# Kernel tuning notes

Measured on AMD Instinct MI355X. Metric: run time of the kernel, lower is better.

The kernel has to match this reference:

```python
import jax, jax.numpy as jnp
import numpy as np
import math

SEQ, BATCH, IN_DIM = 2048, 2, 512
EMBED, HEADS = 512, 8
HEAD_DIM = EMBED // HEADS


def setup_inputs() -> dict:
    key = jax.random.key(0)
    ks = jax.random.split(key, 6)
    # xavier-uniform style init for weights (stored as [in, out])
    def xavier(k, fan_in, fan_out):
        limit = math.sqrt(6.0 / (fan_in + fan_out))
        return jax.random.uniform(k, (fan_in, fan_out), jnp.float32, -limit, limit)
    return {
        "x": jax.random.normal(ks[0], (SEQ, BATCH, IN_DIM), jnp.float32),
        "relative_positional_bias": jax.random.normal(ks[1], (1, HEADS, SEQ, SEQ), jnp.float32),
        "Wqkv": xavier(ks[2], IN_DIM, 3 * EMBED),
        "bqkv": jnp.zeros((3 * EMBED,), jnp.float32),
        "Wo": xavier(ks[3], EMBED, EMBED),
        "bo": jnp.zeros((EMBED,), jnp.float32),
    }


def reference(x, relative_positional_bias, Wqkv, bqkv, Wo, bo):
    # x: [S, B, D] -> [B, S, D]
    xb = jnp.transpose(x, (1, 0, 2))
    B, S, _ = xb.shape
    qkv = xb @ Wqkv + bqkv                       # [B, S, 3E]
    qkv = qkv.reshape(B, S, HEADS, 3 * HEAD_DIM).transpose(0, 2, 1, 3)  # [B,H,S,3hd]
    q, k, v = jnp.split(qkv, 3, axis=-1)         # each [B, H, S, hd]
    # nonstandard scaling: 1/sqrt(2 * d_k)
    scale = 1.0 / math.sqrt(2.0 * HEAD_DIM)
    logits = jnp.einsum("bhqd,bhkd->bhqk", q, k) * scale
    logits = logits + relative_positional_bias   # broadcast over batch
    attn = jax.nn.softmax(logits, axis=-1)
    vals = jnp.einsum("bhqk,bhkd->bhqd", attn, v)  # [B, H, S, hd]
    vals = vals.transpose(0, 2, 1, 3).reshape(B, S, EMBED)
    return vals @ Wo + bo                        # [B, S, E]
```

## Files before the change

### kernel.cpp

```cpp
#include <hip/hip_runtime.h>
#include <hip/hip_bf16.h>

#define SEQ 2048
#define BATCH 2
#define IN_DIM 512
#define EMBED 512
#define HEADS 8
#define HD 64
#define N3 1536

using f32x4 = __attribute__((ext_vector_type(4))) float;
using s16x8 = __attribute__((ext_vector_type(8))) short;

__device__ __forceinline__ unsigned short f2bf(float f) {
    union { float f; unsigned int u; } v; v.f = f;
    unsigned int u = v.u;
    unsigned int r = (u + 0x7FFFu + ((u >> 16) & 1u)) >> 16;
    return (unsigned short)r;
}

__global__ __launch_bounds__(256) void qkv_proj(
    const float* __restrict__ x, const float* __restrict__ Wqkv,
    const float* __restrict__ bqkv,
    unsigned short* __restrict__ Qb, unsigned short* __restrict__ Kb,
    unsigned short* __restrict__ Vt)
{
    __shared__ __align__(16) unsigned short As[64][72];
    __shared__ __align__(16) unsigned short Bs[64][72];
    const int bm = blockIdx.x, bn = blockIdx.y;
    const int tid = threadIdx.x;
    const int lane = tid & 63, w = tid >> 6;
    const int fr = lane & 15, fg = lane >> 4;
    const int m0 = bm * 64, n0 = bn * 64;
    const int ri = tid >> 2;
    const int cj = (tid & 3) * 16;

    f32x4 acc[4];
#pragma unroll
    for (int t = 0; t < 4; t++) acc[t] = (f32x4){0.f, 0.f, 0.f, 0.f};

    const int gm = m0 + ri;
    const int b_ = gm >> 11, s_ = gm & 2047;
    const float* xrow = x + ((size_t)s_ * BATCH + b_) * IN_DIM;

    for (int k0 = 0; k0 < IN_DIM; k0 += 64) {
        {
            const float4* src = reinterpret_cast<const float4*>(xrow + k0 + cj);
#pragma unroll
            for (int v = 0; v < 4; v++) {
                float4 f = src[v];
                ushort4 u;
                u.x = f2bf(f.x); u.y = f2bf(f.y); u.z = f2bf(f.z); u.w = f2bf(f.w);
                *reinterpret_cast<ushort4*>(&As[ri][cj + 4 * v]) = u;
            }
        }
        {
            const float4* src = reinterpret_cast<const float4*>(Wqkv + (size_t)(k0 + ri) * N3 + n0 + cj);
#pragma unroll
            for (int v = 0; v < 4; v++) {
                float4 f = src[v];
                Bs[cj + 4 * v + 0][ri] = f2bf(f.x);
                Bs[cj + 4 * v + 1][ri] = f2bf(f.y);
                Bs[cj + 4 * v + 2][ri] = f2bf(f.z);
                Bs[cj + 4 * v + 3][ri] = f2bf(f.w);
            }
        }
        __syncthreads();
#pragma unroll
        for (int h2 = 0; h2 < 2; h2++) {
            s16x8 a = *reinterpret_cast<const s16x8*>(&As[w * 16 + fr][h2 * 32 + fg * 8]);
#pragma unroll
            for (int t = 0; t < 4; t++) {
                s16x8 b = *reinterpret_cast<const s16x8*>(&Bs[t * 16 + fr][h2 * 32 + fg * 8]);
                acc[t] = __builtin_amdgcn_mfma_f32_16x16x32_bf16(a, b, acc[t], 0, 0, 0);
            }
        }
        __syncthreads();
    }

#pragma unroll
    for (int t = 0; t < 4; t++) {
        const int col = n0 + t * 16 + fr;
        const int h = col / 192, r = col % 192;
        const float bq = bqkv[col];
#pragma unroll
        for (int j = 0; j < 4; j++) {
            const int grow = m0 + w * 16 + fg * 4 + j;
            const int bo_ = grow >> 11, so_ = grow & 2047;
            const unsigned short bv = f2bf(acc[t][j] + bq);
            if (r < 64)
                Qb[(((size_t)bo_ * HEADS + h) * SEQ + so_) * HD + r] = bv;
            else if (r < 128)
                Kb[(((size_t)bo_ * HEADS + h) * SEQ + so_) * HD + (r - 64)] = bv;
            else
                Vt[(((size_t)bo_ * HEADS + h) * HD + (r - 128)) * SEQ + so_] = bv;
        }
    }
}

__global__ __launch_bounds__(256) void flash_attn(
    const unsigned short* __restrict__ Qb, const unsigned short* __restrict__ Kb,
    const unsigned short* __restrict__ Vt, const float* __restrict__ bias,
    unsigned short* __restrict__ Ob)
{
    __shared__ __align__(16) unsigned short Ks[2][64][72];
    __shared__ __align__(16) unsigned short Vs[2][64][72];
    __shared__ __align__(16) unsigned short Ps[4][16][72];
    const int h = blockIdx.y;
    const int q0 = blockIdx.x * 64;
    const int tid = threadIdx.x, lane = tid & 63, w = tid >> 6;
    const int fr = lane & 15, fg = lane >> 4;
    const int ri = tid >> 2, cj = (tid & 3) * 16;

    s16x8 qf[2][2];
#pragma unroll
    for (int b = 0; b < 2; b++) {
        const unsigned short* qrow = Qb + (((size_t)b * HEADS + h) * SEQ + q0 + w * 16 + fr) * HD;
#pragma unroll
        for (int h2 = 0; h2 < 2; h2++)
            qf[b][h2] = *reinterpret_cast<const s16x8*>(qrow + h2 * 32 + fg * 8);
    }

    float mrow[2][4], lrow[2][4];
    f32x4 oacc[2][4];
#pragma unroll
    for (int b = 0; b < 2; b++)
#pragma unroll
        for (int j = 0; j < 4; j++) { mrow[b][j] = -1e30f; lrow[b][j] = 0.f; }
#pragma unroll
    for (int b = 0; b < 2; b++)
#pragma unroll
        for (int t = 0; t < 4; t++) oacc[b][t] = (f32x4){0.f, 0.f, 0.f, 0.f};

    const float scale = 0.08838834764831845f;

    for (int k0 = 0; k0 < SEQ; k0 += 64) {
#pragma unroll
        for (int b = 0; b < 2; b++) {
            const unsigned short* ksrc = Kb + (((size_t)b * HEADS + h) * SEQ + k0 + ri) * HD + cj;
            *reinterpret_cast<uint4*>(&Ks[b][ri][cj])     = *reinterpret_cast<const uint4*>(ksrc);
            *reinterpret_cast<uint4*>(&Ks[b][ri][cj + 8]) = *reinterpret_cast<const uint4*>(ksrc + 8);
            const unsigned short* vsrc = Vt + (((size_t)b * HEADS + h) * HD + ri) * SEQ + k0 + cj;
            *reinterpret_cast<uint4*>(&Vs[b][ri][cj])     = *reinterpret_cast<const uint4*>(vsrc);
            *reinterpret_cast<uint4*>(&Vs[b][ri][cj + 8]) = *reinterpret_cast<const uint4*>(vsrc + 8);
        }
        __syncthreads();

        float biasr[4][4];
#pragma unroll
        for (int t = 0; t < 4; t++)
#pragma unroll
            for (int j = 0; j < 4; j++) {
                const int grow = q0 + w * 16 + fg * 4 + j;
                biasr[t][j] = bias[((size_t)h * SEQ + grow) * SEQ + k0 + t * 16 + fr];
            }

#pragma unroll
        for (int b = 0; b < 2; b++) {
            f32x4 sacc[4];
#pragma unroll
            for (int t = 0; t < 4; t++) sacc[t] = (f32x4){0.f, 0.f, 0.f, 0.f};
#pragma unroll
            for (int h2 = 0; h2 < 2; h2++) {
                s16x8 a = qf[b][h2];
#pragma unroll
                for (int t = 0; t < 4; t++) {
                    s16x8 kf = *reinterpret_cast<const s16x8*>(&Ks[b][t * 16 + fr][h2 * 32 + fg * 8]);
                    sacc[t] = __builtin_amdgcn_mfma_f32_16x16x32_bf16(a, kf, sacc[t], 0, 0, 0);
                }
            }
#pragma unroll
            for (int t = 0; t < 4; t++)
#pragma unroll
                for (int j = 0; j < 4; j++)
                    sacc[t][j] = sacc[t][j] * scale + biasr[t][j];
            float fac[4];
#pragma unroll
            for (int j = 0; j < 4; j++) {
                float m = fmaxf(fmaxf(sacc[0][j], sacc[1][j]), fmaxf(sacc[2][j], sacc[3][j]));
#pragma unroll
                for (int msk = 1; msk < 16; msk <<= 1) m = fmaxf(m, __shfl_xor(m, msk, 64));
                const float newm = fmaxf(mrow[b][j], m);
                fac[j] = __expf(mrow[b][j] - newm);
                mrow[b][j] = newm;
            }
#pragma unroll
            for (int t = 0; t < 4; t++)
#pragma unroll
                for (int j = 0; j < 4; j++)
                    sacc[t][j] = __expf(sacc[t][j] - mrow[b][j]);
#pragma unroll
            for (int j = 0; j < 4; j++) {
                float s = sacc[0][j] + sacc[1][j] + sacc[2][j] + sacc[3][j];
#pragma unroll
                for (int msk = 1; msk < 16; msk <<= 1) s += __shfl_xor(s, msk, 64);
                lrow[b][j] = lrow[b][j] * fac[j] + s;
            }
#pragma unroll
            for (int t = 0; t < 4; t++)
#pragma unroll
                for (int j = 0; j < 4; j++)
                    Ps[w][fg * 4 + j][t * 16 + fr] = f2bf(sacc[t][j]);
#pragma unroll
            for (int t = 0; t < 4; t++)
#pragma unroll
                for (int j = 0; j < 4; j++)
                    oacc[b][t][j] *= fac[j];
#pragma unroll
            for (int h2 = 0; h2 < 2; h2++) {
                s16x8 pa = *reinterpret_cast<const s16x8*>(&Ps[w][fr][h2 * 32 + fg * 8]);
#pragma unroll
                for (int t = 0; t < 4; t++) {
                    s16x8 vf = *reinterpret_cast<const s16x8*>(&Vs[b][t * 16 + fr][h2 * 32 + fg * 8]);
                    oacc[b][t] = __builtin_amdgcn_mfma_f32_16x16x32_bf16(pa, vf, oacc[b][t], 0, 0, 0);
                }
            }
        }
        __syncthreads();
    }

#pragma unroll
    for (int b = 0; b < 2; b++)
#pragma unroll
        for (int t = 0; t < 4; t++)
#pragma unroll
            for (int j = 0; j < 4; j++) {
                const int grow = q0 + w * 16 + fg * 4 + j;
                const float o = oacc[b][t][j] / lrow[b][j];
                Ob[((size_t)b * SEQ + grow) * EMBED + h * HD + t * 16 + fr] = f2bf(o);
            }
}

__global__ __launch_bounds__(256) void out_proj(
    const unsigned short* __restrict__ Ao, const float* __restrict__ Wo,
    const float* __restrict__ bo, float* __restrict__ out)
{
    __shared__ __align__(16) unsigned short As[64][72];
    __shared__ __align__(16) unsigned short Bs[64][72];
    const int bm = blockIdx.x, bn = blockIdx.y;
    const int tid = threadIdx.x, lane = tid & 63, w = tid >> 6;
    const int fr = lane & 15, fg = lane >> 4;
    const int m0 = bm * 64, n0 = bn * 64;
    const int ri = tid >> 2, cj = (tid & 3) * 16;

    f32x4 acc[4];
#pragma unroll
    for (int t = 0; t < 4; t++) acc[t] = (f32x4){0.f, 0.f, 0.f, 0.f};

    for (int k0 = 0; k0 < EMBED; k0 += 64) {
        const unsigned short* asrc = Ao + (size_t)(m0 + ri) * EMBED + k0 + cj;
        *reinterpret_cast<uint4*>(&As[ri][cj])     = *reinterpret_cast<const uint4*>(asrc);
        *reinterpret_cast<uint4*>(&As[ri][cj + 8]) = *reinterpret_cast<const uint4*>(asrc + 8);
        const float4* bsrc = reinterpret_cast<const float4*>(Wo + (size_t)(k0 + ri) * EMBED + n0 + cj);
#pragma unroll
        for (int v = 0; v < 4; v++) {
            float4 f = bsrc[v];
            Bs[cj + 4 * v + 0][ri] = f2bf(f.x);
            Bs[cj + 4 * v + 1][ri] = f2bf(f.y);
            Bs[cj + 4 * v + 2][ri] = f2bf(f.z);
            Bs[cj + 4 * v + 3][ri] = f2bf(f.w);
        }
        __syncthreads();
#pragma unroll
        for (int h2 = 0; h2 < 2; h2++) {
            s16x8 a = *reinterpret_cast<const s16x8*>(&As[w * 16 + fr][h2 * 32 + fg * 8]);
#pragma unroll
            for (int t = 0; t < 4; t++) {
                s16x8 b = *reinterpret_cast<const s16x8*>(&Bs[t * 16 + fr][h2 * 32 + fg * 8]);
                acc[t] = __builtin_amdgcn_mfma_f32_16x16x32_bf16(a, b, acc[t], 0, 0, 0);
            }
        }
        __syncthreads();
    }

#pragma unroll
    for (int t = 0; t < 4; t++) {
        const int col = n0 + t * 16 + fr;
        const float bb = bo[col];
#pragma unroll
        for (int j = 0; j < 4; j++) {
            const int grow = m0 + w * 16 + fg * 4 + j;
            out[(size_t)grow * EMBED + col] = acc[t][j] + bb;
        }
    }
}

extern "C" void kernel_launch(void* const* d_in, const int* in_sizes, int n_in,
                              void* d_out, int out_size, void* d_ws, size_t ws_size,
                              hipStream_t stream) {
    const float* x    = (const float*)d_in[0];
    const float* bias = (const float*)d_in[1];
    const float* Wqkv = (const float*)d_in[2];
    const float* bqkv = (const float*)d_in[3];
    const float* Wo   = (const float*)d_in[4];
    const float* bo   = (const float*)d_in[5];
    float* out = (float*)d_out;

    const size_t perT = (size_t)BATCH * HEADS * SEQ * HD;
    unsigned short* Qb = (unsigned short*)d_ws;
    unsigned short* Kb = Qb + perT;
    unsigned short* Vt = Kb + perT;
    unsigned short* Ob = Vt + perT;

    qkv_proj<<<dim3(64, 24), 256, 0, stream>>>(x, Wqkv, bqkv, Qb, Kb, Vt);
    flash_attn<<<dim3(32, 8), 256, 0, stream>>>(Qb, Kb, Vt, bias, Ob);
    out_proj<<<dim3(64, 8), 256, 0, stream>>>(Ob, Wo, bo, out);
}
```

Before: 319.4 us.

## Precast inputs to bf16, pipeline flash attention, split batch across blocks

```diff
diff --git a/kernel.cpp b/kernel.cpp
--- a/kernel.cpp
+++ b/kernel.cpp
@@ -19,8 +19,42 @@
     return (unsigned short)r;
 }
 
+__global__ __launch_bounds__(256) void prep_x(
+    const float* __restrict__ x, unsigned short* __restrict__ Ab)
+{
+    const int gid = blockIdx.x * 256 + threadIdx.x;
+    const int base = gid * 4;
+    const int m = base >> 9, k = base & 511;
+    const int b = m >> 11, s = m & 2047;
+    float4 f = *reinterpret_cast<const float4*>(x + ((size_t)s * BATCH + b) * IN_DIM + k);
+    ushort4 u;
+    u.x = f2bf(f.x); u.y = f2bf(f.y); u.z = f2bf(f.z); u.w = f2bf(f.w);
+    *reinterpret_cast<ushort4*>(Ab + (size_t)m * IN_DIM + k) = u;
+}
+
+__global__ __launch_bounds__(256) void transpose_w(
+    const float* __restrict__ in, unsigned short* __restrict__ out, int K, int N)
+{
+    __shared__ __align__(16) unsigned short T[64][72];
+    const int k0 = blockIdx.x * 64, n0 = blockIdx.y * 64;
+    const int tid = threadIdx.x;
+    const int ri = tid >> 2, cj = (tid & 3) * 16;
+#pragma unroll
+    for (int v = 0; v < 4; v++) {
+        float4 f = *reinterpret_cast<const float4*>(in + (size_t)(k0 + ri) * N + n0 + cj + 4 * v);
+        T[cj + 4 * v + 0][ri] = f2bf(f.x);
+        T[cj + 4 * v + 1][ri] = f2bf(f.y);
+        T[cj + 4 * v + 2][ri] = f2bf(f.z);
+        T[cj + 4 * v + 3][ri] = f2bf(f.w);
+    }
+    __syncthreads();
+    unsigned short* dst = out + (size_t)(n0 + ri) * K + k0 + cj;
+    *reinterpret_cast<uint4*>(dst)     = *reinterpret_cast<const uint4*>(&T[ri][cj]);
+    *reinterpret_cast<uint4*>(dst + 8) = *reinterpret_cast<const uint4*>(&T[ri][cj + 8]);
+}
+
 __global__ __launch_bounds__(256) void qkv_proj(
-    const float* __restrict__ x, const float* __restrict__ Wqkv,
+    const unsigned short* __restrict__ Ab, const unsigned short* __restrict__ Wt,
     const float* __restrict__ bqkv,
     unsigned short* __restrict__ Qb, unsigned short* __restrict__ Kb,
     unsigned short* __restrict__ Vt)
@@ -32,39 +66,19 @@
     const int lane = tid & 63, w = tid >> 6;
     const int fr = lane & 15, fg = lane >> 4;
     const int m0 = bm * 64, n0 = bn * 64;
-    const int ri = tid >> 2;
-    const int cj = (tid & 3) * 16;
+    const int ri = tid >> 2, cj = (tid & 3) * 16;
 
     f32x4 acc[4];
 #pragma unroll
     for (int t = 0; t < 4; t++) acc[t] = (f32x4){0.f, 0.f, 0.f, 0.f};
 
-    const int gm = m0 + ri;
-    const int b_ = gm >> 11, s_ = gm & 2047;
-    const float* xrow = x + ((size_t)s_ * BATCH + b_) * IN_DIM;
-
     for (int k0 = 0; k0 < IN_DIM; k0 += 64) {
-        {
-            const float4* src = reinterpret_cast<const float4*>(xrow + k0 + cj);
-#pragma unroll
-            for (int v = 0; v < 4; v++) {
-                float4 f = src[v];
-                ushort4 u;
-                u.x = f2bf(f.x); u.y = f2bf(f.y); u.z = f2bf(f.z); u.w = f2bf(f.w);
-                *reinterpret_cast<ushort4*>(&As[ri][cj + 4 * v]) = u;
-            }
-        }
-        {
-            const float4* src = reinterpret_cast<const float4*>(Wqkv + (size_t)(k0 + ri) * N3 + n0 + cj);
-#pragma unroll
-            for (int v = 0; v < 4; v++) {
-                float4 f = src[v];
-                Bs[cj + 4 * v + 0][ri] = f2bf(f.x);
-                Bs[cj + 4 * v + 1][ri] = f2bf(f.y);
-                Bs[cj + 4 * v + 2][ri] = f2bf(f.z);
-                Bs[cj + 4 * v + 3][ri] = f2bf(f.w);
-            }
-        }
+        const unsigned short* asrc = Ab + (size_t)(m0 + ri) * IN_DIM + k0 + cj;
+        *reinterpret_cast<uint4*>(&As[ri][cj])     = *reinterpret_cast<const uint4*>(asrc);
+        *reinterpret_cast<uint4*>(&As[ri][cj + 8]) = *reinterpret_cast<const uint4*>(asrc + 8);
+        const unsigned short* bsrc = Wt + (size_t)(n0 + ri) * IN_DIM + k0 + cj;
+        *reinterpret_cast<uint4*>(&Bs[ri][cj])     = *reinterpret_cast<const uint4*>(bsrc);
+        *reinterpret_cast<uint4*>(&Bs[ri][cj + 8]) = *reinterpret_cast<const uint4*>(bsrc + 8);
         __syncthreads();
 #pragma unroll
         for (int h2 = 0; h2 < 2; h2++) {
@@ -78,23 +92,32 @@
         __syncthreads();
     }
 
-#pragma unroll
-    for (int t = 0; t < 4; t++) {
-        const int col = n0 + t * 16 + fr;
-        const int h = col / 192, r = col % 192;
-        const float bq = bqkv[col];
-#pragma unroll
-        for (int j = 0; j < 4; j++) {
-            const int grow = m0 + w * 16 + fg * 4 + j;
-            const int bo_ = grow >> 11, so_ = grow & 2047;
-            const unsigned short bv = f2bf(acc[t][j] + bq);
-            if (r < 64)
-                Qb[(((size_t)bo_ * HEADS + h) * SEQ + so_) * HD + r] = bv;
-            else if (r < 128)
-                Kb[(((size_t)bo_ * HEADS + h) * SEQ + so_) * HD + (r - 64)] = bv;
-            else
-                Vt[(((size_t)bo_ * HEADS + h) * HD + (r - 128)) * SEQ + so_] = bv;
-        }
+    const int h = bn / 3, route = bn % 3;
+    const int b_ = m0 >> 11, s0 = m0 & 2047;
+    if (route < 2) {
+        unsigned short* dst = (route == 0) ? Qb : Kb;
+#pragma unroll
+        for (int t = 0; t < 4; t++) {
+            const int d = t * 16 + fr;
+            const float bq = bqkv[n0 + t * 16 + fr];
+#pragma unroll
+            for (int j = 0; j < 4; j++) {
+                const int sl = s0 + w * 16 + fg * 4 + j;
+                dst[(((size_t)b_ * HEADS + h) * SEQ + sl) * HD + d] = f2bf(acc[t][j] + bq);
+            }
+        }
+    } else {
+#pragma unroll
+        for (int t = 0; t < 4; t++) {
+            const float bq = bqkv[n0 + t * 16 + fr];
+#pragma unroll
+            for (int j = 0; j < 4; j++)
+                As[t * 16 + fr][w * 16 + fg * 4 + j] = f2bf(acc[t][j] + bq);
+        }
+        __syncthreads();
+        unsigned short* dst = Vt + (((size_t)b_ * HEADS + h) * HD + ri) * SEQ + s0 + cj;
+        *reinterpret_cast<uint4*>(dst)     = *reinterpret_cast<const uint4*>(&As[ri][cj]);
+        *reinterpret_cast<uint4*>(dst + 8) = *reinterpret_cast<const uint4*>(&As[ri][cj + 8]);
     }
 }
 
@@ -106,133 +129,149 @@
     __shared__ __align__(16) unsigned short Ks[2][64][72];
     __shared__ __align__(16) unsigned short Vs[2][64][72];
     __shared__ __align__(16) unsigned short Ps[4][16][72];
-    const int h = blockIdx.y;
+    const int h = blockIdx.y, b = blockIdx.z;
     const int q0 = blockIdx.x * 64;
     const int tid = threadIdx.x, lane = tid & 63, w = tid >> 6;
     const int fr = lane & 15, fg = lane >> 4;
-    const int ri = tid >> 2, cj = (tid & 3) * 16;
-
-    s16x8 qf[2][2];
-#pragma unroll
-    for (int b = 0; b < 2; b++) {
-        const unsigned short* qrow = Qb + (((size_t)b * HEADS + h) * SEQ + q0 + w * 16 + fr) * HD;
-#pragma unroll
-        for (int h2 = 0; h2 < 2; h2++)
-            qf[b][h2] = *reinterpret_cast<const s16x8*>(qrow + h2 * 32 + fg * 8);
-    }
-
-    float mrow[2][4], lrow[2][4];
-    f32x4 oacc[2][4];
-#pragma unroll
-    for (int b = 0; b < 2; b++)
-#pragma unroll
-        for (int j = 0; j < 4; j++) { mrow[b][j] = -1e30f; lrow[b][j] = 0.f; }
-#pragma unroll
-    for (int b = 0; b < 2; b++)
-#pragma unroll
-        for (int t = 0; t < 4; t++) oacc[b][t] = (f32x4){0.f, 0.f, 0.f, 0.f};
+
+    const unsigned short* Kbase = Kb + (size_t)(b * HEADS + h) * SEQ * HD;
+    const unsigned short* Vbase = Vt + (size_t)(b * HEADS + h) * HD * SEQ;
+    const float* bbase = bias + (size_t)h * SEQ * SEQ + (size_t)q0 * SEQ;
+
+    const unsigned short* qrow = Qb + ((size_t)(b * HEADS + h) * SEQ + q0 + w * 16 + fr) * HD;
+    s16x8 qf0 = *reinterpret_cast<const s16x8*>(qrow + fg * 8);
+    s16x8 qf1 = *reinterpret_cast<const s16x8*>(qrow + 32 + fg * 8);
+
+    const int r0 = tid >> 3, c0 = (tid & 7) * 8;
+    const int r1 = r0 + 32;
+
+    uint4 kr0, kr1, vr0, vr1;
+    float bA[4][4], bB[4][4];
+
+    kr0 = *reinterpret_cast<const uint4*>(Kbase + (size_t)r0 * HD + c0);
+    kr1 = *reinterpret_cast<const uint4*>(Kbase + (size_t)r1 * HD + c0);
+    vr0 = *reinterpret_cast<const uint4*>(Vbase + (size_t)r0 * SEQ + c0);
+    vr1 = *reinterpret_cast<const uint4*>(Vbase + (size_t)r1 * SEQ + c0);
+#pragma unroll
+    for (int t = 0; t < 4; t++)
+#pragma unroll
+        for (int j = 0; j < 4; j++)
+            bA[t][j] = bbase[(size_t)(w * 16 + fg * 4 + j) * SEQ + t * 16 + fr];
+    *reinterpret_cast<uint4*>(&Ks[0][r0][c0]) = kr0;
+    *reinterpret_cast<uint4*>(&Ks[0][r1][c0]) = kr1;
+    *reinterpret_cast<uint4*>(&Vs[0][r0][c0]) = vr0;
+    *reinterpret_cast<uint4*>(&Vs[0][r1][c0]) = vr1;
+    __syncthreads();
+
+    float mrow[4], lrow[4];
+    f32x4 oacc[4];
+#pragma unroll
+    for (int j = 0; j < 4; j++) { mrow[j] = -1e30f; lrow[j] = 0.f; }
+#pragma unroll
+    for (int t = 0; t < 4; t++) oacc[t] = (f32x4){0.f, 0.f, 0.f, 0.f};
 
     const float scale = 0.08838834764831845f;
 
-    for (int k0 = 0; k0 < SEQ; k0 += 64) {
-#pragma unroll
-        for (int b = 0; b < 2; b++) {
-            const unsigned short* ksrc = Kb + (((size_t)b * HEADS + h) * SEQ + k0 + ri) * HD + cj;
-            *reinterpret_cast<uint4*>(&Ks[b][ri][cj])     = *reinterpret_cast<const uint4*>(ksrc);
-            *reinterpret_cast<uint4*>(&Ks[b][ri][cj + 8]) = *reinterpret_cast<const uint4*>(ksrc + 8);
-            const unsigned short* vsrc = Vt + (((size_t)b * HEADS + h) * HD + ri) * SEQ + k0 + cj;
-            *reinterpret_cast<uint4*>(&Vs[b][ri][cj])     = *reinterpret_cast<const uint4*>(vsrc);
-            *reinterpret_cast<uint4*>(&Vs[b][ri][cj + 8]) = *reinterpret_cast<const uint4*>(vsrc + 8);
-        }
-        __syncthreads();
-
-        float biasr[4][4];
+    auto body = [&](int n, const float (&bc)[4][4], float (&bnx)[4][4]) {
+        const int cur = n & 1;
+        const bool pf = (n < 31);
+        const int kn = (n + 1) * 64;
+        if (pf) {
+            kr0 = *reinterpret_cast<const uint4*>(Kbase + (size_t)(kn + r0) * HD + c0);
+            kr1 = *reinterpret_cast<const uint4*>(Kbase + (size_t)(kn + r1) * HD + c0);
+            vr0 = *reinterpret_cast<const uint4*>(Vbase + (size_t)r0 * SEQ + kn + c0);
+            vr1 = *reinterpret_cast<const uint4*>(Vbase + (size_t)r1 * SEQ + kn + c0);
+#pragma unroll
+            for (int t = 0; t < 4; t++)
+#pragma unroll
+                for (int j = 0; j < 4; j++)
+                    bnx[t][j] = bbase[(size_t)(w * 16 + fg * 4 + j) * SEQ + kn + t * 16 + fr];
+        }
+        f32x4 sacc[4];
+#pragma unroll
+        for (int t = 0; t < 4; t++) sacc[t] = (f32x4){0.f, 0.f, 0.f, 0.f};
+#pragma unroll
+        for (int h2 = 0; h2 < 2; h2++) {
+            s16x8 a = (h2 == 0) ? qf0 : qf1;
+#pragma unroll
+            for (int t = 0; t < 4; t++) {
+                s16x8 kf = *reinterpret_cast<const s16x8*>(&Ks[cur][t * 16 + fr][h2 * 32 + fg * 8]);
+                sacc[t] = __builtin_amdgcn_mfma_f32_16x16x32_bf16(a, kf, sacc[t], 0, 0, 0);
+            }
+        }
 #pragma unroll
         for (int t = 0; t < 4; t++)
 #pragma unroll
-            for (int j = 0; j < 4; j++) {
-                const int grow = q0 + w * 16 + fg * 4 + j;
-                biasr[t][j] = bias[((size_t)h * SEQ + grow) * SEQ + k0 + t * 16 + fr];
-            }
-
-#pragma unroll
-        for (int b = 0; b < 2; b++) {
-            f32x4 sacc[4];
-#pragma unroll
-            for (int t = 0; t < 4; t++) sacc[t] = (f32x4){0.f, 0.f, 0.f, 0.f};
-#pragma unroll
-            for (int h2 = 0; h2 < 2; h2++) {
-                s16x8 a = qf[b][h2];
-#pragma unroll
-                for (int t = 0; t < 4; t++) {
-                    s16x8 kf = *reinterpret_cast<const s16x8*>(&Ks[b][t * 16 + fr][h2 * 32 + fg * 8]);
-                    sacc[t] = __builtin_amdgcn_mfma_f32_16x16x32_bf16(a, kf, sacc[t], 0, 0, 0);
-                }
-            }
-#pragma unroll
-            for (int t = 0; t < 4; t++)
-#pragma unroll
-                for (int j = 0; j < 4; j++)
-                    sacc[t][j] = sacc[t][j] * scale + biasr[t][j];
-            float fac[4];
-#pragma unroll
-            for (int j = 0; j < 4; j++) {
-                float m = fmaxf(fmaxf(sacc[0][j], sacc[1][j]), fmaxf(sacc[2][j], sacc[3][j]));
-#pragma unroll
-                for (int msk = 1; msk < 16; msk <<= 1) m = fmaxf(m, __shfl_xor(m, msk, 64));
-                const float newm = fmaxf(mrow[b][j], m);
-                fac[j] = __expf(mrow[b][j] - newm);
-                mrow[b][j] = newm;
-            }
-#pragma unroll
-            for (int t = 0; t < 4; t++)
-#pragma unroll
-                for (int j = 0; j < 4; j++)
-                    sacc[t][j] = __expf(sacc[t][j] - mrow[b][j]);
-#pragma unroll
-            for (int j = 0; j < 4; j++) {
-                float s = sacc[0][j] + sacc[1][j] + sacc[2][j] + sacc[3][j];
-#pragma unroll
-                for (int msk = 1; msk < 16; msk <<= 1) s += __shfl_xor(s, msk, 64);
-                lrow[b][j] = lrow[b][j] * fac[j] + s;
-            }
-#pragma unroll
-            for (int t = 0; t < 4; t++)
-#pragma unroll
-                for (int j = 0; j < 4; j++)
-                    Ps[w][fg * 4 + j][t * 16 + fr] = f2bf(sacc[t][j]);
-#pragma unroll
-            for (int t = 0; t < 4; t++)
-#pragma unroll
-                for (int j = 0; j < 4; j++)
-                    oacc[b][t][j] *= fac[j];
-#pragma unroll
-            for (int h2 = 0; h2 < 2; h2++) {
-                s16x8 pa = *reinterpret_cast<const s16x8*>(&Ps[w][fr][h2 * 32 + fg * 8]);
-#pragma unroll
-                for (int t = 0; t < 4; t++) {
-                    s16x8 vf = *reinterpret_cast<const s16x8*>(&Vs[b][t * 16 + fr][h2 * 32 + fg * 8]);
-                    oacc[b][t] = __builtin_amdgcn_mfma_f32_16x16x32_bf16(pa, vf, oacc[b][t], 0, 0, 0);
-                }
-            }
-        }
-        __syncthreads();
-    }
-
-#pragma unroll
-    for (int b = 0; b < 2; b++)
+            for (int j = 0; j < 4; j++)
+                sacc[t][j] = sacc[t][j] * scale + bc[t][j];
+        float fac[4];
+#pragma unroll
+        for (int j = 0; j < 4; j++) {
+            float m = fmaxf(fmaxf(sacc[0][j], sacc[1][j]), fmaxf(sacc[2][j], sacc[3][j]));
+#pragma unroll
+            for (int msk = 1; msk < 16; msk <<= 1) m = fmaxf(m, __shfl_xor(m, msk, 64));
+            const float newm = fmaxf(mrow[j], m);
+            fac[j] = __expf(mrow[j] - newm);
+            mrow[j] = newm;
+        }
 #pragma unroll
         for (int t = 0; t < 4; t++)
 #pragma unroll
-            for (int j = 0; j < 4; j++) {
-                const int grow = q0 + w * 16 + fg * 4 + j;
-                const float o = oacc[b][t][j] / lrow[b][j];
-                Ob[((size_t)b * SEQ + grow) * EMBED + h * HD + t * 16 + fr] = f2bf(o);
-            }
+            for (int j = 0; j < 4; j++)
+                sacc[t][j] = __expf(sacc[t][j] - mrow[j]);
+#pragma unroll
+        for (int j = 0; j < 4; j++) {
+            float s = sacc[0][j] + sacc[1][j] + sacc[2][j] + sacc[3][j];
+#pragma unroll
+            for (int msk = 1; msk < 16; msk <<= 1) s += __shfl_xor(s, msk, 64);
+            lrow[j] = lrow[j] * fac[j] + s;
+        }
+#pragma unroll
+        for (int t = 0; t < 4; t++)
+#pragma unroll
+            for (int j = 0; j < 4; j++)
+                Ps[w][fg * 4 + j][t * 16 + fr] = f2bf(sacc[t][j]);
+#pragma unroll
+        for (int t = 0; t < 4; t++)
+#pragma unroll
+            for (int j = 0; j < 4; j++)
+                oacc[t][j] *= fac[j];
+#pragma unroll
+        for (int h2 = 0; h2 < 2; h2++) {
+            s16x8 pa = *reinterpret_cast<const s16x8*>(&Ps[w][fr][h2 * 32 + fg * 8]);
+#pragma unroll
+            for (int t = 0; t < 4; t++) {
+                s16x8 vf = *reinterpret_cast<const s16x8*>(&Vs[cur][t * 16 + fr][h2 * 32 + fg * 8]);
+                oacc[t] = __builtin_amdgcn_mfma_f32_16x16x32_bf16(pa, vf, oacc[t], 0, 0, 0);
+            }
+        }
+        if (pf) {
+            const int nxt = cur ^ 1;
+            *reinterpret_cast<uint4*>(&Ks[nxt][r0][c0]) = kr0;
+            *reinterpret_cast<uint4*>(&Ks[nxt][r1][c0]) = kr1;
+            *reinterpret_cast<uint4*>(&Vs[nxt][r0][c0]) = vr0;
+            *reinterpret_cast<uint4*>(&Vs[nxt][r1][c0]) = vr1;
+        }
+        __syncthreads();
+    };
+
+    for (int n = 0; n < 32; n += 2) {
+        body(n, bA, bB);
+        body(n + 1, bB, bA);
+    }
+
+#pragma unroll
+    for (int t = 0; t < 4; t++)
+#pragma unroll
+        for (int j = 0; j < 4; j++) {
+            const int grow = q0 + w * 16 + fg * 4 + j;
+            const float o = oacc[t][j] / lrow[j];
+            Ob[((size_t)b * SEQ + grow) * EMBED + h * HD + t * 16 + fr] = f2bf(o);
+        }
 }
 
 __global__ __launch_bounds__(256) void out_proj(
-    const unsigned short* __restrict__ Ao, const float* __restrict__ Wo,
+    const unsigned short* __restrict__ Ao, const unsigned short* __restrict__ Wot,
     const float* __restrict__ bo, float* __restrict__ out)
 {
     __shared__ __align__(16) unsigned short As[64][72];
@@ -251,15 +290,9 @@
         const unsigned short* asrc = Ao + (size_t)(m0 + ri) * EMBED + k0 + cj;
         *reinterpret_cast<uint4*>(&As[ri][cj])     = *reinterpret_cast<const uint4*>(asrc);
         *reinterpret_cast<uint4*>(&As[ri][cj + 8]) = *reinterpret_cast<const uint4*>(asrc + 8);
-        const float4* bsrc = reinterpret_cast<const float4*>(Wo + (size_t)(k0 + ri) * EMBED + n0 + cj);
-#pragma unroll
-        for (int v = 0; v < 4; v++) {
-            float4 f = bsrc[v];
-            Bs[cj + 4 * v + 0][ri] = f2bf(f.x);
-            Bs[cj + 4 * v + 1][ri] = f2bf(f.y);
-            Bs[cj + 4 * v + 2][ri] = f2bf(f.z);
-            Bs[cj + 4 * v + 3][ri] = f2bf(f.w);
-        }
+        const unsigned short* bsrc = Wot + (size_t)(n0 + ri) * EMBED + k0 + cj;
+        *reinterpret_cast<uint4*>(&Bs[ri][cj])     = *reinterpret_cast<const uint4*>(bsrc);
+        *reinterpret_cast<uint4*>(&Bs[ri][cj + 8]) = *reinterpret_cast<const uint4*>(bsrc + 8);
         __syncthreads();
 #pragma unroll
         for (int h2 = 0; h2 < 2; h2++) {
@@ -297,12 +330,18 @@
     float* out = (float*)d_out;
 
     const size_t perT = (size_t)BATCH * HEADS * SEQ * HD;
-    unsigned short* Qb = (unsigned short*)d_ws;
-    unsigned short* Kb = Qb + perT;
-    unsigned short* Vt = Kb + perT;
-    unsigned short* Ob = Vt + perT;
-
-    qkv_proj<<<dim3(64, 24), 256, 0, stream>>>(x, Wqkv, bqkv, Qb, Kb, Vt);
-    flash_attn<<<dim3(32, 8), 256, 0, stream>>>(Qb, Kb, Vt, bias, Ob);
-    out_proj<<<dim3(64, 8), 256, 0, stream>>>(Ob, Wo, bo, out);
-}
+    unsigned short* Qb    = (unsigned short*)d_ws;
+    unsigned short* Kb    = Qb + perT;
+    unsigned short* Vt    = Kb + perT;
+    unsigned short* Ob    = Vt + perT;
+    unsigned short* Ab    = Ob + perT;
+    unsigned short* Wqkvt = Ab + (size_t)BATCH * SEQ * IN_DIM;
+    unsigned short* Wot   = Wqkvt + (size_t)N3 * IN_DIM;
+
+    prep_x<<<2048, 256, 0, stream>>>(x, Ab);
+    transpose_w<<<dim3(8, 24), 256, 0, stream>>>(Wqkv, Wqkvt, IN_DIM, N3);
+    transpose_w<<<dim3(8, 8), 256, 0, stream>>>(Wo, Wot, EMBED, EMBED);
+    qkv_proj<<<dim3(64, 24), 256, 0, stream>>>(Ab, Wqkvt, bqkv, Qb, Kb, Vt);
+    flash_attn<<<dim3(32, 8, 2), 256, 0, stream>>>(Qb, Kb, Vt, bias, Ob);
+    out_proj<<<dim3(64, 8), 256, 0, stream>>>(Ob, Wot, bo, out);
+}
```

After: 266.1 us. -16.7%, faster.
